# Kernel optimization log

Measured on AMD Instinct MI355X. Metric: run time of the kernel, lower is better.

The kernel has to match this reference:

```python
import jax, jax.numpy as jnp
import numpy as np

N_NODES = 50000
N_EDGES = 800000
IN_DIM = 128
HID = 64
HEADS = 4
OUT = 16
N_GRAPHS = 500
NEG_SLOPE = 0.2


def setup_inputs() -> dict:
    key = jax.random.key(0)
    ks = jax.random.split(key, 12)
    x = jax.random.normal(ks[0], (N_NODES, IN_DIM), dtype=jnp.float32)
    edge_index = jax.random.randint(ks[1], (2, N_EDGES), 0, N_NODES, dtype=jnp.int64)
    batch = jnp.sort(jax.random.randint(ks[2], (N_NODES,), 0, N_GRAPHS, dtype=jnp.int64))
    s1 = 1.0 / np.sqrt(IN_DIM)
    s2 = 1.0 / np.sqrt(HID)
    W1 = jax.random.normal(ks[3], (IN_DIM, HEADS * HID), dtype=jnp.float32) * s1
    a1_src = jax.random.normal(ks[4], (HEADS, HID), dtype=jnp.float32) * s2
    a1_dst = jax.random.normal(ks[5], (HEADS, HID), dtype=jnp.float32) * s2
    b1 = jnp.zeros((HID,), dtype=jnp.float32)
    W2 = jax.random.normal(ks[6], (HID, HEADS * HID), dtype=jnp.float32) * s2
    a2_src = jax.random.normal(ks[7], (HEADS, HID), dtype=jnp.float32) * s2
    a2_dst = jax.random.normal(ks[8], (HEADS, HID), dtype=jnp.float32) * s2
    b2 = jnp.zeros((HID,), dtype=jnp.float32)
    fcW = jax.random.normal(ks[9], (HID, OUT), dtype=jnp.float32) * s2
    fcb = jnp.zeros((OUT,), dtype=jnp.float32)
    return {"x": x, "edge_index": edge_index, "batch": batch,
            "W1": W1, "a1_src": a1_src, "a1_dst": a1_dst, "b1": b1,
            "W2": W2, "a2_src": a2_src, "a2_dst": a2_dst, "b2": b2,
            "fcW": fcW, "fcb": fcb}


def gat_conv(x, W, a_src, a_dst, b, src, dst):
    # PyG GATConv with concat=False: per-head linear, edge softmax over dst, head-mean.
    n = x.shape[0]
    h = (x @ W).reshape(n, HEADS, HID)          # [N,H,D]
    alpha_s = jnp.sum(h * a_src, axis=-1)        # [N,H]
    alpha_d = jnp.sum(h * a_dst, axis=-1)        # [N,H]
    e = jax.nn.leaky_relu(alpha_s[src] + alpha_d[dst], NEG_SLOPE)  # [E,H]
    emax = jax.ops.segment_max(e, dst, num_segments=n)
    ex = jnp.exp(e - emax[dst])
    denom = jax.ops.segment_sum(ex, dst, num_segments=n)
    alpha = ex / denom[dst]                      # [E,H], edge softmax per dst
    msg = h[src] * alpha[:, :, None]             # [E,H,D]
    out = jax.ops.segment_sum(msg, dst, num_segments=n)  # [N,H,D]
    return out.mean(axis=1) + b                  # concat=False -> head mean


def reference(x, edge_index, batch, W1, a1_src, a1_dst, b1, W2, a2_src, a2_dst, b2, fcW, fcb):
    n = x.shape[0]
    # PyG GATConv default add_self_loops=True
    loops = jnp.arange(n, dtype=edge_index.dtype)
    src = jnp.concatenate([edge_index[0], loops])
    dst = jnp.concatenate([edge_index[1], loops])
    h = jax.nn.relu(gat_conv(x, W1, a1_src, a1_dst, b1, src, dst))
    h = jax.nn.relu(gat_conv(h, W2, a2_src, a2_dst, b2, src, dst))
    # global_mean_pool over batch ids
    sums = jax.ops.segment_sum(h, batch, num_segments=N_GRAPHS)
    counts = jax.ops.segment_sum(jnp.ones((n,), dtype=h.dtype), batch, num_segments=N_GRAPHS)
    pooled = sums / jnp.clip(counts, 1.0)[:, None]
    return pooled @ fcW + fcb
```

## Files before the change

### kernel.cpp

```cpp
#include <hip/hip_runtime.h>
#include <hip/hip_bf16.h>
#include <hip/hip_fp16.h>

#define NN 50000
#define EE 800000
#define ETOT 850000
#define NG 500
#define NBLK ((NN + 255) / 256)

__global__ void k_detect(const int* __restrict__ ei, int* __restrict__ flag) {
    unsigned long long b = __ballot(ei[2 * threadIdx.x + 1] != 0);
    if (threadIdx.x == 0) *flag = b ? 1 : 2;
}

__global__ __launch_bounds__(256) void k_prep(const int* __restrict__ ei,
                                              const int* __restrict__ flag,
                                              int* __restrict__ src32,
                                              int* __restrict__ dst32,
                                              int* __restrict__ deg) {
    int e = blockIdx.x * 256 + threadIdx.x;
    if (e >= ETOT) return;
    int st = *flag;
    int s, d;
    if (e < EE) {
        s = ei[(size_t)st * e];
        d = ei[(size_t)st * (EE + e)];
    } else {
        s = d = e - EE;
    }
    src32[e] = s;
    dst32[e] = d;
    atomicAdd(&deg[d], 1);
}

__global__ __launch_bounds__(256) void k_blocksum(const int* __restrict__ deg,
                                                  int* __restrict__ bsum) {
    __shared__ int l[256];
    int gid = blockIdx.x * 256 + threadIdx.x;
    int tid = threadIdx.x;
    l[tid] = (gid < NN) ? deg[gid] : 0;
    __syncthreads();
    for (int o = 128; o > 0; o >>= 1) {
        if (tid < o) l[tid] += l[tid + o];
        __syncthreads();
    }
    if (tid == 0) bsum[blockIdx.x] = l[0];
}

__global__ __launch_bounds__(256) void k_scan_bsum(const int* __restrict__ bsum,
                                                   int* __restrict__ boff) {
    __shared__ int l[256];
    int tid = threadIdx.x;
    int v = (tid < NBLK) ? bsum[tid] : 0;
    l[tid] = v;
    __syncthreads();
    for (int d = 1; d < 256; d <<= 1) {
        int t = (tid >= d) ? l[tid - d] : 0;
        __syncthreads();
        l[tid] += t;
        __syncthreads();
    }
    if (tid < NBLK) boff[tid] = l[tid] - v;
}

__global__ __launch_bounds__(256) void k_scan_final(const int* __restrict__ deg,
                                                    const int* __restrict__ boff,
                                                    int* __restrict__ rowptr,
                                                    int* __restrict__ cursor) {
    __shared__ int l[256];
    int gid = blockIdx.x * 256 + threadIdx.x;
    int tid = threadIdx.x;
    int v = (gid < NN) ? deg[gid] : 0;
    l[tid] = v;
    __syncthreads();
    for (int d = 1; d < 256; d <<= 1) {
        int t = (tid >= d) ? l[tid - d] : 0;
        __syncthreads();
        l[tid] += t;
        __syncthreads();
    }
    int ex = l[tid] - v + boff[blockIdx.x];
    if (gid < NN) { rowptr[gid] = ex; cursor[gid] = ex; }
    if (gid == 0) rowptr[NN] = ETOT;
}

__global__ __launch_bounds__(256) void k_scatter(const int* __restrict__ src32,
                                                 const int* __restrict__ dst32,
                                                 int* __restrict__ cursor,
                                                 int* __restrict__ csr_src) {
    int e = blockIdx.x * 256 + threadIdx.x;
    if (e >= ETOT) return;
    int pos = atomicAdd(&cursor[dst32[e]], 1);
    csr_src[pos] = src32[e];
}

template <int K>
__global__ __launch_bounds__(256) void k_gemm(const float* __restrict__ A,
                                              const float* __restrict__ B,
                                              const float* __restrict__ asrc,
                                              const float* __restrict__ adst,
                                              __half* __restrict__ C16,
                                              float* __restrict__ os,
                                              float* __restrict__ od, int M) {
    __shared__ float As[16][34];
    __shared__ float Bs[16][260];
    const int m0 = blockIdx.x * 32;
    const int tid = threadIdx.x;
    const int tx = tid & 15, ty = tid >> 4;
    float acc[2][16] = {};
    for (int k0 = 0; k0 < K; k0 += 16) {
        {
            int r = tid >> 3, c = (tid & 7) * 2;
            int gm = m0 + r;
            float2 av = (gm < M) ? *(const float2*)(A + gm * K + k0 + c)
                                 : make_float2(0.f, 0.f);
            As[c][r] = av.x;
            As[c + 1][r] = av.y;
        }
        {
            int col = (tid & 63) * 4, rb = tid >> 6;
#pragma unroll
            for (int p = 0; p < 4; ++p) {
                int row = p * 4 + rb;
                *(float4*)&Bs[row][col] = *(const float4*)(B + (k0 + row) * 256 + col);
            }
        }
        __syncthreads();
#pragma unroll
        for (int k = 0; k < 16; ++k) {
            float a0 = As[k][ty * 2], a1 = As[k][ty * 2 + 1];
            float b[16];
#pragma unroll
            for (int h = 0; h < 4; ++h)
                *(float4*)&b[h * 4] = *(const float4*)&Bs[k][h * 64 + tx * 4];
#pragma unroll
            for (int j = 0; j < 16; ++j) {
                acc[0][j] += a0 * b[j];
                acc[1][j] += a1 * b[j];
            }
        }
        __syncthreads();
    }
#pragma unroll
    for (int i = 0; i < 2; ++i) {
        int gm = m0 + ty * 2 + i;
        if (gm < M) {
            __half hbuf[16];
#pragma unroll
            for (int jd = 0; jd < 4; ++jd) {
                __half2 p0 = __floats2half2_rn(acc[i][0 * 4 + jd], acc[i][1 * 4 + jd]);
                __half2 p1 = __floats2half2_rn(acc[i][2 * 4 + jd], acc[i][3 * 4 + jd]);
                *(__half2*)&hbuf[jd * 4]     = p0;
                *(__half2*)&hbuf[jd * 4 + 2] = p1;
            }
            *(uint4*)(C16 + gm * 256 + tx * 16)     = *(uint4*)&hbuf[0];
            *(uint4*)(C16 + gm * 256 + tx * 16 + 8) = *(uint4*)&hbuf[8];
        }
    }
    float ps[2][4], pd[2][4];
#pragma unroll
    for (int h = 0; h < 4; ++h) {
        float4 av = *(const float4*)&asrc[h * 64 + tx * 4];
        float4 dv = *(const float4*)&adst[h * 64 + tx * 4];
#pragma unroll
        for (int i = 0; i < 2; ++i) {
            ps[i][h] = acc[i][h * 4 + 0] * av.x + acc[i][h * 4 + 1] * av.y +
                       acc[i][h * 4 + 2] * av.z + acc[i][h * 4 + 3] * av.w;
            pd[i][h] = acc[i][h * 4 + 0] * dv.x + acc[i][h * 4 + 1] * dv.y +
                       acc[i][h * 4 + 2] * dv.z + acc[i][h * 4 + 3] * dv.w;
        }
    }
#pragma unroll
    for (int off = 1; off < 16; off <<= 1) {
#pragma unroll
        for (int i = 0; i < 2; ++i)
#pragma unroll
            for (int h = 0; h < 4; ++h) {
                ps[i][h] += __shfl_xor(ps[i][h], off);
                pd[i][h] += __shfl_xor(pd[i][h], off);
            }
    }
    if (tx == 0) {
#pragma unroll
        for (int i = 0; i < 2; ++i) {
            int gm = m0 + ty * 2 + i;
            if (gm < M) {
                *(float4*)(os + gm * 4) = make_float4(ps[i][0], ps[i][1], ps[i][2], ps[i][3]);
                *(float4*)(od + gm * 4) = make_float4(pd[i][0], pd[i][1], pd[i][2], pd[i][3]);
            }
        }
    }
}

__device__ __forceinline__ float lrelu_exp(float x) {
    x = x > 0.f ? x : 0.2f * x;
    return __expf(x);
}

__global__ __launch_bounds__(256) void k_aggr(const int* __restrict__ rowptr,
                                              const int* __restrict__ csr_src,
                                              const float* __restrict__ as_,
                                              const float* __restrict__ ad_,
                                              const __half* __restrict__ h16,
                                              const float* __restrict__ bias,
                                              float* __restrict__ out) {
    int d = (blockIdx.x * 256 + threadIdx.x) >> 6;
    int lane = threadIdx.x & 63;
    if (d >= NN) return;
    int beg = rowptr[d], end = rowptr[d + 1];
    float4 adv = *(const float4*)(ad_ + d * 4);

    int s0 = 0;
    float4 u0 = make_float4(0.f, 0.f, 0.f, 0.f);
    float4 den = make_float4(0.f, 0.f, 0.f, 0.f);
    int i0 = beg + lane;
    if (i0 < end) {
        s0 = csr_src[i0];
        float4 sv = *(const float4*)(as_ + s0 * 4);
        u0.x = lrelu_exp(sv.x + adv.x);
        u0.y = lrelu_exp(sv.y + adv.y);
        u0.z = lrelu_exp(sv.z + adv.z);
        u0.w = lrelu_exp(sv.w + adv.w);
        den = u0;
    }
    for (int i = i0 + 64; i < end; i += 64) {
        int s = csr_src[i];
        float4 sv = *(const float4*)(as_ + s * 4);
        den.x += lrelu_exp(sv.x + adv.x);
        den.y += lrelu_exp(sv.y + adv.y);
        den.z += lrelu_exp(sv.z + adv.z);
        den.w += lrelu_exp(sv.w + adv.w);
    }
#pragma unroll
    for (int off = 32; off > 0; off >>= 1) {
        den.x += __shfl_xor(den.x, off);
        den.y += __shfl_xor(den.y, off);
        den.z += __shfl_xor(den.z, off);
        den.w += __shfl_xor(den.w, off);
    }
    float4 dinv = make_float4(0.25f / den.x, 0.25f / den.y,
                              0.25f / den.z, 0.25f / den.w);

    float4 al0 = make_float4(u0.x * dinv.x, u0.y * dinv.y,
                             u0.z * dinv.z, u0.w * dinv.w);
    int cnt = end - beg;
    if (cnt > 64) cnt = 64;
    int cnt4 = (cnt + 3) & ~3;
    float acc = 0.f;
    uint2 r0, r1, r2, r3;
    {
        int sa = __shfl(s0, 0), sb = __shfl(s0, 1);
        int sc = __shfl(s0, 2), sd = __shfl(s0, 3);
        r0 = *(const uint2*)(h16 + (size_t)sa * 256 + lane * 4);
        r1 = *(const uint2*)(h16 + (size_t)sb * 256 + lane * 4);
        r2 = *(const uint2*)(h16 + (size_t)sc * 256 + lane * 4);
        r3 = *(const uint2*)(h16 + (size_t)sd * 256 + lane * 4);
    }
    for (int j = 0; j < cnt4; j += 4) {
        int sa = __shfl(s0, (j + 4) & 63), sb = __shfl(s0, (j + 5) & 63);
        int sc = __shfl(s0, (j + 6) & 63), sd = __shfl(s0, (j + 7) & 63);
        uint2 n0 = *(const uint2*)(h16 + (size_t)sa * 256 + lane * 4);
        uint2 n1 = *(const uint2*)(h16 + (size_t)sb * 256 + lane * 4);
        uint2 n2 = *(const uint2*)(h16 + (size_t)sc * 256 + lane * 4);
        uint2 n3 = *(const uint2*)(h16 + (size_t)sd * 256 + lane * 4);
        float a00 = __shfl(al0.x, j),     a01 = __shfl(al0.y, j),     a02 = __shfl(al0.z, j),     a03 = __shfl(al0.w, j);
        float a10 = __shfl(al0.x, j + 1), a11 = __shfl(al0.y, j + 1), a12 = __shfl(al0.z, j + 1), a13 = __shfl(al0.w, j + 1);
        float a20 = __shfl(al0.x, j + 2), a21 = __shfl(al0.y, j + 2), a22 = __shfl(al0.z, j + 2), a23 = __shfl(al0.w, j + 2);
        float a30 = __shfl(al0.x, j + 3), a31 = __shfl(al0.y, j + 3), a32 = __shfl(al0.z, j + 3), a33 = __shfl(al0.w, j + 3);
        float2 fa, fb;
        fa = __half22float2(*(const __half2*)&r0.x);
        fb = __half22float2(*(const __half2*)&r0.y);
        acc += a00 * fa.x + a01 * fa.y + a02 * fb.x + a03 * fb.y;
        fa = __half22float2(*(const __half2*)&r1.x);
        fb = __half22float2(*(const __half2*)&r1.y);
        acc += a10 * fa.x + a11 * fa.y + a12 * fb.x + a13 * fb.y;
        fa = __half22float2(*(const __half2*)&r2.x);
        fb = __half22float2(*(const __half2*)&r2.y);
        acc += a20 * fa.x + a21 * fa.y + a22 * fb.x + a23 * fb.y;
        fa = __half22float2(*(const __half2*)&r3.x);
        fb = __half22float2(*(const __half2*)&r3.y);
        acc += a30 * fa.x + a31 * fa.y + a32 * fb.x + a33 * fb.y;
        r0 = n0; r1 = n1; r2 = n2; r3 = n3;
    }
    for (int chunk = beg + 64; chunk < end; chunk += 64) {
        int i = chunk + lane;
        int s = 0;
        float4 al = make_float4(0.f, 0.f, 0.f, 0.f);
        if (i < end) {
            s = csr_src[i];
            float4 sv = *(const float4*)(as_ + s * 4);
            al.x = lrelu_exp(sv.x + adv.x) * dinv.x;
            al.y = lrelu_exp(sv.y + adv.y) * dinv.y;
            al.z = lrelu_exp(sv.z + adv.z) * dinv.z;
            al.w = lrelu_exp(sv.w + adv.w) * dinv.w;
        }
        int cc = end - chunk;
        if (cc > 64) cc = 64;
        for (int j = 0; j < cc; ++j) {
            int sj = __shfl(s, j);
            float a0 = __shfl(al.x, j), a1 = __shfl(al.y, j);
            float a2 = __shfl(al.z, j), a3 = __shfl(al.w, j);
            uint2 raw = *(const uint2*)(h16 + (size_t)sj * 256 + lane * 4);
            float2 fa = __half22float2(*(const __half2*)&raw.x);
            float2 fb = __half22float2(*(const __half2*)&raw.y);
            acc += a0 * fa.x + a1 * fa.y + a2 * fb.x + a3 * fb.y;
        }
    }
    float v = acc + bias[lane];
    out[d * 64 + lane] = v > 0.f ? v : 0.f;
}

__global__ __launch_bounds__(256) void k_pool_fc(const float* __restrict__ x3,
                                                 const int* __restrict__ batch,
                                                 const int* __restrict__ flag,
                                                 const float* __restrict__ fcW,
                                                 const float* __restrict__ fcb,
                                                 float* __restrict__ out) {
    int g = blockIdx.x;
    int tid = threadIdx.x, lane = tid & 63, w = tid >> 6;
    int st = *flag;
    int lo = 0, hi = NN;
    while (lo < hi) { int mid = (lo + hi) >> 1; if (batch[(size_t)st * mid] < g) lo = mid + 1; else hi = mid; }
    int start = lo;
    hi = NN;
    while (lo < hi) { int mid = (lo + hi) >> 1; if (batch[(size_t)st * mid] < g + 1) lo = mid + 1; else hi = mid; }
    int end = lo;
    float sum = 0.f;
    for (int n = start + w; n < end; n += 4) sum += x3[n * 64 + lane];
    __shared__ float ls[4][64];
    ls[w][lane] = sum;
    __syncthreads();
    if (w == 0) {
        float c = (float)(end - start);
        if (c < 1.f) c = 1.f;
        float p = (ls[0][lane] + ls[1][lane] + ls[2][lane] + ls[3][lane]) / c;
#pragma unroll
        for (int o = 0; o < 16; ++o) {
            float v = p * fcW[lane * 16 + o];
#pragma unroll
            for (int off = 32; off > 0; off >>= 1) v += __shfl_down(v, off);
            if (lane == 0) out[g * 16 + o] = v + fcb[o];
        }
    }
}

extern "C" void kernel_launch(void* const* d_in, const int* in_sizes, int n_in,
                              void* d_out, int out_size, void* d_ws, size_t ws_size,
                              hipStream_t stream) {
    const float* x   = (const float*)d_in[0];
    const int*   ei  = (const int*)d_in[1];
    const int*   bat = (const int*)d_in[2];
    const float* W1  = (const float*)d_in[3];
    const float* a1s = (const float*)d_in[4];
    const float* a1d = (const float*)d_in[5];
    const float* b1  = (const float*)d_in[6];
    const float* W2  = (const float*)d_in[7];
    const float* a2s = (const float*)d_in[8];
    const float* a2d = (const float*)d_in[9];
    const float* b2  = (const float*)d_in[10];
    const float* fcW = (const float*)d_in[11];
    const float* fcb = (const float*)d_in[12];
    float* out = (float*)d_out;

    float* ws = (float*)d_ws;
    int* flag = (int*)d_ws;
    __half* h16  = (__half*)(ws + 256);
    float* as_   = (float*)(h16 + (size_t)NN * 256);
    float* ad_   = as_ + NN * 4;
    float* xacc  = ad_ + NN * 4;
    int* src32   = (int*)(xacc + (size_t)NN * 64);
    int* dst32   = src32 + ETOT;
    int* deg     = dst32 + ETOT;
    int* rowptr  = deg + NN;
    int* cursor  = rowptr + NN + 1;
    int* csr_src = cursor + NN;
    int* bsum    = csr_src + ETOT;
    int* boff    = bsum + NBLK;

    const int eb = (ETOT + 255) / 256;
    const int wb = (NN * 64 + 255) / 256;

    k_detect<<<1, 64, 0, stream>>>(ei, flag);
    hipMemsetAsync(deg, 0, NN * sizeof(int), stream);
    k_prep<<<eb, 256, 0, stream>>>(ei, flag, src32, dst32, deg);
    k_blocksum<<<NBLK, 256, 0, stream>>>(deg, bsum);
    k_scan_bsum<<<1, 256, 0, stream>>>(bsum, boff);
    k_scan_final<<<NBLK, 256, 0, stream>>>(deg, boff, rowptr, cursor);
    k_scatter<<<eb, 256, 0, stream>>>(src32, dst32, cursor, csr_src);

    const int gg = (NN + 31) / 32;
    k_gemm<128><<<gg, 256, 0, stream>>>(x, W1, a1s, a1d, h16, as_, ad_, NN);
    k_aggr<<<wb, 256, 0, stream>>>(rowptr, csr_src, as_, ad_, h16, b1, xacc);
    k_gemm<64><<<gg, 256, 0, stream>>>(xacc, W2, a2s, a2d, h16, as_, ad_, NN);
    k_aggr<<<wb, 256, 0, stream>>>(rowptr, csr_src, as_, ad_, h16, b2, xacc);
    k_pool_fc<<<NG, 256, 0, stream>>>(xacc, bat, flag, fcW, fcb, out);
}
```

Measured before the change: 435.3 us.

## Replace FP32 SIMT GEMMs with split-bf16 MFMA GEMMs using pre-permuted weights

The scalar FP32 tiled GEMM is replaced by a matrix-core kernel using 16x16x32 bf16 MFMA. Each FP32 operand is split into high and low bf16 parts, and three MFMAs (hi·hi, hi·lo, lo·hi) recover near-FP32 accuracy. A new pre-pass kernel transposes and splits the weights and permutes the columns and attention vectors to match the existing h16 layout. The attention dot-products are now computed from the MFMA accumulators with lane shuffles. This trades the FMA-bound SIMT GEMM for matrix-core throughput, at the cost of extra MFMAs, two small prep launches, and narrower, more scattered half-precision stores.

```diff
diff --git a/kernel.cpp b/kernel.cpp
--- a/kernel.cpp
+++ b/kernel.cpp
@@ -7,6 +7,15 @@
 #define ETOT 850000
 #define NG 500
 #define NBLK ((NN + 255) / 256)
+
+typedef __attribute__((ext_vector_type(8))) short bf16x8;
+typedef __attribute__((ext_vector_type(4))) float f32x4;
+
+__device__ __forceinline__ unsigned short bf16_rne(float v) {
+    unsigned u = __float_as_uint(v);
+    unsigned r = u + 0x7FFFu + ((u >> 16) & 1u);
+    return (unsigned short)(r >> 16);
+}
 
 __global__ void k_detect(const int* __restrict__ ei, int* __restrict__ flag) {
     unsigned long long b = __ballot(ei[2 * threadIdx.x + 1] != 0);
@@ -95,99 +104,92 @@
 }
 
 template <int K>
-__global__ __launch_bounds__(256) void k_gemm(const float* __restrict__ A,
-                                              const float* __restrict__ B,
-                                              const float* __restrict__ asrc,
-                                              const float* __restrict__ adst,
-                                              __half* __restrict__ C16,
-                                              float* __restrict__ os,
-                                              float* __restrict__ od, int M) {
-    __shared__ float As[16][34];
-    __shared__ float Bs[16][260];
-    const int m0 = blockIdx.x * 32;
-    const int tid = threadIdx.x;
-    const int tx = tid & 15, ty = tid >> 4;
-    float acc[2][16] = {};
-    for (int k0 = 0; k0 < K; k0 += 16) {
-        {
-            int r = tid >> 3, c = (tid & 7) * 2;
-            int gm = m0 + r;
-            float2 av = (gm < M) ? *(const float2*)(A + gm * K + k0 + c)
-                                 : make_float2(0.f, 0.f);
-            As[c][r] = av.x;
-            As[c + 1][r] = av.y;
-        }
-        {
-            int col = (tid & 63) * 4, rb = tid >> 6;
-#pragma unroll
-            for (int p = 0; p < 4; ++p) {
-                int row = p * 4 + rb;
-                *(float4*)&Bs[row][col] = *(const float4*)(B + (k0 + row) * 256 + col);
-            }
-        }
-        __syncthreads();
-#pragma unroll
-        for (int k = 0; k < 16; ++k) {
-            float a0 = As[k][ty * 2], a1 = As[k][ty * 2 + 1];
-            float b[16];
-#pragma unroll
-            for (int h = 0; h < 4; ++h)
-                *(float4*)&b[h * 4] = *(const float4*)&Bs[k][h * 64 + tx * 4];
-#pragma unroll
-            for (int j = 0; j < 16; ++j) {
-                acc[0][j] += a0 * b[j];
-                acc[1][j] += a1 * b[j];
-            }
-        }
-        __syncthreads();
-    }
-#pragma unroll
-    for (int i = 0; i < 2; ++i) {
-        int gm = m0 + ty * 2 + i;
-        if (gm < M) {
-            __half hbuf[16];
-#pragma unroll
-            for (int jd = 0; jd < 4; ++jd) {
-                __half2 p0 = __floats2half2_rn(acc[i][0 * 4 + jd], acc[i][1 * 4 + jd]);
-                __half2 p1 = __floats2half2_rn(acc[i][2 * 4 + jd], acc[i][3 * 4 + jd]);
-                *(__half2*)&hbuf[jd * 4]     = p0;
-                *(__half2*)&hbuf[jd * 4 + 2] = p1;
-            }
-            *(uint4*)(C16 + gm * 256 + tx * 16)     = *(uint4*)&hbuf[0];
-            *(uint4*)(C16 + gm * 256 + tx * 16 + 8) = *(uint4*)&hbuf[8];
-        }
-    }
-    float ps[2][4], pd[2][4];
-#pragma unroll
-    for (int h = 0; h < 4; ++h) {
-        float4 av = *(const float4*)&asrc[h * 64 + tx * 4];
-        float4 dv = *(const float4*)&adst[h * 64 + tx * 4];
-#pragma unroll
-        for (int i = 0; i < 2; ++i) {
-            ps[i][h] = acc[i][h * 4 + 0] * av.x + acc[i][h * 4 + 1] * av.y +
-                       acc[i][h * 4 + 2] * av.z + acc[i][h * 4 + 3] * av.w;
-            pd[i][h] = acc[i][h * 4 + 0] * dv.x + acc[i][h * 4 + 1] * dv.y +
-                       acc[i][h * 4 + 2] * dv.z + acc[i][h * 4 + 3] * dv.w;
-        }
-    }
-#pragma unroll
-    for (int off = 1; off < 16; off <<= 1) {
-#pragma unroll
-        for (int i = 0; i < 2; ++i)
-#pragma unroll
-            for (int h = 0; h < 4; ++h) {
-                ps[i][h] += __shfl_xor(ps[i][h], off);
-                pd[i][h] += __shfl_xor(pd[i][h], off);
-            }
-    }
-    if (tx == 0) {
-#pragma unroll
-        for (int i = 0; i < 2; ++i) {
-            int gm = m0 + ty * 2 + i;
-            if (gm < M) {
-                *(float4*)(os + gm * 4) = make_float4(ps[i][0], ps[i][1], ps[i][2], ps[i][3]);
-                *(float4*)(od + gm * 4) = make_float4(pd[i][0], pd[i][1], pd[i][2], pd[i][3]);
-            }
+__global__ __launch_bounds__(256) void k_prepw(const float* __restrict__ W,
+                                               const float* __restrict__ asrc,
+                                               const float* __restrict__ adst,
+                                               unsigned short* __restrict__ bhi,
+                                               unsigned short* __restrict__ blo,
+                                               float* __restrict__ aperm,
+                                               float* __restrict__ adperm) {
+    int t = blockIdx.x * 256 + threadIdx.x;
+    int j = t / K, k = t - j * K;
+    int d = j >> 2, h = j & 3;
+    float v = W[k * 256 + h * 64 + d];
+    unsigned short hb = bf16_rne(v);
+    float hf = __uint_as_float((unsigned)hb << 16);
+    bhi[t] = hb;
+    blo[t] = bf16_rne(v - hf);
+    if (k == 0) { aperm[j] = asrc[h * 64 + d]; adperm[j] = adst[h * 64 + d]; }
+}
+
+template <int K>
+__global__ __launch_bounds__(256) void k_gemm_mfma(
+        const float* __restrict__ A,
+        const unsigned short* __restrict__ Bhi,
+        const unsigned short* __restrict__ Blo,
+        const float* __restrict__ aperm,
+        const float* __restrict__ adperm,
+        __half* __restrict__ C16,
+        float* __restrict__ os,
+        float* __restrict__ od, int M) {
+    const int NC = K / 32;
+    int wave = threadIdx.x >> 6;
+    int lane = threadIdx.x & 63;
+    int l = lane & 15, q = lane >> 4;
+    int m0 = blockIdx.x * 64 + wave * 16;
+    if (m0 >= M) return;
+
+    bf16x8 ahi[NC], alo[NC];
+    const float* arow = A + (size_t)(m0 + l) * K + q * 8;
+#pragma unroll
+    for (int c = 0; c < NC; ++c) {
+        float4 v0 = *(const float4*)(arow + c * 32);
+        float4 v1 = *(const float4*)(arow + c * 32 + 4);
+        float vv[8] = {v0.x, v0.y, v0.z, v0.w, v1.x, v1.y, v1.z, v1.w};
+#pragma unroll
+        for (int j = 0; j < 8; ++j) {
+            unsigned short hb = bf16_rne(vv[j]);
+            float hf = __uint_as_float((unsigned)hb << 16);
+            ahi[c][j] = (short)hb;
+            alo[c][j] = (short)bf16_rne(vv[j] - hf);
+        }
+    }
+
+    float ps[4] = {0.f, 0.f, 0.f, 0.f}, pd[4] = {0.f, 0.f, 0.f, 0.f};
+    const size_t brow = (size_t)l * K + q * 8;
+#pragma unroll 2
+    for (int n = 0; n < 16; ++n) {
+        f32x4 acc = {0.f, 0.f, 0.f, 0.f};
+        const unsigned short* bh = Bhi + (size_t)(n * 16) * K + brow;
+        const unsigned short* bl = Blo + (size_t)(n * 16) * K + brow;
+#pragma unroll
+        for (int c = 0; c < NC; ++c) {
+            bf16x8 bhf = *(const bf16x8*)(bh + c * 32);
+            bf16x8 blf = *(const bf16x8*)(bl + c * 32);
+            acc = __builtin_amdgcn_mfma_f32_16x16x32_bf16(ahi[c], bhf, acc, 0, 0, 0);
+            acc = __builtin_amdgcn_mfma_f32_16x16x32_bf16(ahi[c], blf, acc, 0, 0, 0);
+            acc = __builtin_amdgcn_mfma_f32_16x16x32_bf16(alo[c], bhf, acc, 0, 0, 0);
+        }
+        float av = aperm[n * 16 + l], dv = adperm[n * 16 + l];
+#pragma unroll
+        for (int r = 0; r < 4; ++r) {
+            ps[r] += acc[r] * av;
+            pd[r] += acc[r] * dv;
+            C16[(size_t)(m0 + q * 4 + r) * 256 + n * 16 + l] = __float2half(acc[r]);
+        }
+    }
+#pragma unroll
+    for (int r = 0; r < 4; ++r) {
+        ps[r] += __shfl_xor(ps[r], 4);
+        ps[r] += __shfl_xor(ps[r], 8);
+        pd[r] += __shfl_xor(pd[r], 4);
+        pd[r] += __shfl_xor(pd[r], 8);
+    }
+    if (l < 4) {
+#pragma unroll
+        for (int r = 0; r < 4; ++r) {
+            os[(size_t)(m0 + q * 4 + r) * 4 + l] = ps[r];
+            od[(size_t)(m0 + q * 4 + r) * 4 + l] = pd[r];
         }
     }
 }
@@ -376,6 +378,16 @@
     int* csr_src = cursor + NN;
     int* bsum    = csr_src + ETOT;
     int* boff    = bsum + NBLK;
+    char* p = (char*)(boff + NBLK);
+    p = (char*)(((size_t)p + 255) & ~(size_t)255);
+    unsigned short* bt1h = (unsigned short*)p; p += 256 * 128 * 2;
+    unsigned short* bt1l = (unsigned short*)p; p += 256 * 128 * 2;
+    unsigned short* bt2h = (unsigned short*)p; p += 256 * 64 * 2;
+    unsigned short* bt2l = (unsigned short*)p; p += 256 * 64 * 2;
+    float* ap1  = (float*)p; p += 256 * 4;
+    float* adp1 = (float*)p; p += 256 * 4;
+    float* ap2  = (float*)p; p += 256 * 4;
+    float* adp2 = (float*)p; p += 256 * 4;
 
     const int eb = (ETOT + 255) / 256;
     const int wb = (NN * 64 + 255) / 256;
@@ -383,15 +395,17 @@
     k_detect<<<1, 64, 0, stream>>>(ei, flag);
     hipMemsetAsync(deg, 0, NN * sizeof(int), stream);
     k_prep<<<eb, 256, 0, stream>>>(ei, flag, src32, dst32, deg);
+    k_prepw<128><<<128, 256, 0, stream>>>(W1, a1s, a1d, bt1h, bt1l, ap1, adp1);
+    k_prepw<64><<<64, 256, 0, stream>>>(W2, a2s, a2d, bt2h, bt2l, ap2, adp2);
     k_blocksum<<<NBLK, 256, 0, stream>>>(deg, bsum);
     k_scan_bsum<<<1, 256, 0, stream>>>(bsum, boff);
     k_scan_final<<<NBLK, 256, 0, stream>>>(deg, boff, rowptr, cursor);
     k_scatter<<<eb, 256, 0, stream>>>(src32, dst32, cursor, csr_src);
 
-    const int gg = (NN + 31) / 32;
-    k_gemm<128><<<gg, 256, 0, stream>>>(x, W1, a1s, a1d, h16, as_, ad_, NN);
+    const int gg = (NN + 63) / 64;
+    k_gemm_mfma<128><<<gg, 256, 0, stream>>>(x, bt1h, bt1l, ap1, adp1, h16, as_, ad_, NN);
     k_aggr<<<wb, 256, 0, stream>>>(rowptr, csr_src, as_, ad_, h16, b1, xacc);
-    k_gemm<64><<<gg, 256, 0, stream>>>(xacc, W2, a2s, a2d, h16, as_, ad_, NN);
+    k_gemm_mfma<64><<<gg, 256, 0, stream>>>(xacc, bt2h, bt2l, ap2, adp2, h16, as_, ad_, NN);
     k_aggr<<<wb, 256, 0, stream>>>(rowptr, csr_src, as_, ad_, h16, b2, xacc);
     k_pool_fc<<<NG, 256, 0, stream>>>(xacc, bat, flag, fcW, fcb, out);
 }
```

Result: slower. 444.7 us (+2.2%).
